# Optimization experiments

Measured on AMD Instinct MI355X. Metric: run time of the kernel, lower is better.

Reference implementation:

```python
import jax, jax.numpy as jnp
import numpy as np

D_MODEL = 1024
N_HEADS = 16
SEQ_LEN = 2048
BATCH = 2
NEG = -1.0e9


def sinusoidal_embeddings(seq_len, d_k):
    # Faithful to the torch version: row 0 is all zeros; even cols get sin,
    # odd cols get cos of position/theta (theta uses the SAME index j, not j//2).
    theta = 10000.0 ** (2.0 * jnp.arange(d_k, dtype=jnp.float32) / d_k)  # [d_k]
    pos = jnp.arange(1, seq_len, dtype=jnp.float32)[:, None] / theta      # [S-1, d_k]
    even = (jnp.arange(d_k) % 2 == 0)
    body = jnp.where(even, jnp.sin(pos), jnp.cos(pos))                    # [S-1, d_k]
    return jnp.concatenate([jnp.zeros((1, d_k), dtype=pos.dtype), body], axis=0)


def setup_inputs() -> dict:
    key = jax.random.key(0)
    k_x, k_q, k_k, k_v, k_o = jax.random.split(key, 5)
    scale = 0.02
    return {
        "X": jax.random.normal(k_x, (BATCH, SEQ_LEN, D_MODEL), dtype=jnp.float32),
        "W_q": jax.random.normal(k_q, (D_MODEL, D_MODEL), dtype=jnp.float32) * scale,
        "W_k": jax.random.normal(k_k, (D_MODEL, D_MODEL), dtype=jnp.float32) * scale,
        "W_v": jax.random.normal(k_v, (D_MODEL, D_MODEL), dtype=jnp.float32) * scale,
        "W_o": jax.random.normal(k_o, (D_MODEL, D_MODEL), dtype=jnp.float32) * scale,
    }


def reference(X, W_q, W_k, W_v, W_o):
    B, S, D = X.shape
    H, d_k = N_HEADS, D // N_HEADS

    def proj(W):  # nn.Linear (no bias): y = x @ W.T, then split heads -> [B,H,S,d_k]
        return (X @ W.T).reshape(B, S, H, d_k).transpose(0, 2, 1, 3)

    Q, K, V = proj(W_q), proj(W_k), proj(W_v)

    pos = sinusoidal_embeddings(S, d_k)          # [S, d_k]
    Q = Q + pos
    K = K + pos

    mask = jnp.triu(jnp.full((S, S), NEG, dtype=X.dtype), k=1)  # [S,S]
    scores = jnp.einsum("bhqd,bhkd->bhqk", Q, K) / jnp.sqrt(jnp.float32(d_k)) + mask
    weights = jax.nn.softmax(scores, axis=-1)
    attn = jnp.einsum("bhqk,bhkd->bhqd", weights, V)            # [B,H,S,d_k]

    attn = attn.transpose(0, 2, 1, 3).reshape(B, S, D)
    return attn @ W_o.T + X
```

## Files before the change

kernel.cpp:

```cpp
#include <hip/hip_runtime.h>
#include <hip/hip_bf16.h>
#include <math.h>

#define S_LEN 2048
#define DMODEL 1024
#define NHEADS 16
#define DHEAD 64
#define NBATCH 2
#define MROWS (NBATCH * S_LEN)

typedef float f32x4 __attribute__((ext_vector_type(4)));
typedef unsigned short u16x8 __attribute__((ext_vector_type(8)));
typedef __bf16 bf16x8 __attribute__((ext_vector_type(8)));

__device__ __forceinline__ f32x4 mfma16(u16x8 a, u16x8 b, f32x4 c) {
    return __builtin_amdgcn_mfma_f32_16x16x32_bf16(
        __builtin_bit_cast(bf16x8, a), __builtin_bit_cast(bf16x8, b), c, 0, 0, 0);
}

__device__ __forceinline__ unsigned short f2bf(float f) {
    unsigned int u = __builtin_bit_cast(unsigned int, f);
    u += 0x7FFFu + ((u >> 16) & 1u);
    return (unsigned short)(u >> 16);
}

__device__ __forceinline__ unsigned int cvtpk(float lo, float hi) {
    unsigned int r;
    asm("v_cvt_pk_bf16_f32 %0, %1, %2" : "=v"(r) : "v"(lo), "v"(hi));
    return r;
}

__device__ __forceinline__ void gl16(const void* g, void* l) {
    __builtin_amdgcn_global_load_lds(
        (const __attribute__((address_space(1))) unsigned int*)g,
        (__attribute__((address_space(3))) unsigned int*)l, 16, 0, 0);
}

#define PIPE_BAR_12() do { \
    asm volatile("s_waitcnt vmcnt(12)" ::: "memory"); \
    __builtin_amdgcn_sched_barrier(0); \
    __builtin_amdgcn_s_barrier(); \
    __builtin_amdgcn_sched_barrier(0); } while (0)
#define PIPE_BAR_0() do { \
    asm volatile("s_waitcnt vmcnt(0)" ::: "memory"); \
    __builtin_amdgcn_sched_barrier(0); \
    __builtin_amdgcn_s_barrier(); \
    __builtin_amdgcn_sched_barrier(0); } while (0)

__global__ __launch_bounds__(256) void cvt5(
    const float* __restrict__ X, const float* __restrict__ Wq,
    const float* __restrict__ Wk, const float* __restrict__ Wv,
    const float* __restrict__ Wo,
    unsigned short* __restrict__ Xbf, unsigned short* __restrict__ Wbf,
    float* __restrict__ pos)
{
    int b = blockIdx.x;
    if (b >= 4096) {
        int i = (b - 4096) * 256 + threadIdx.x;
        int s = i >> 6, d = i & 63;
        float theta = powf(10000.0f, (2.0f * (float)d) / 64.0f);
        float x = (float)s / theta;
        float v = (d & 1) ? cosf(x) : sinf(x);
        pos[i] = (s == 0) ? 0.0f : v;
        return;
    }
    const float* s; unsigned short* d; int t;
    if (b < 2048) { s = X; d = Xbf; t = b * 256 + threadIdx.x; }
    else {
        int z = (b - 2048) >> 9, bb = (b - 2048) & 511;
        s = (z == 0) ? Wq : (z == 1) ? Wk : (z == 2) ? Wv : Wo;
        d = Wbf + (z << 20);
        t = bb * 256 + threadIdx.x;
    }
    float4 a = *((const float4*)s + t * 2);
    float4 c = *((const float4*)s + t * 2 + 1);
    u16x8 o;
    o[0] = f2bf(a.x); o[1] = f2bf(a.y); o[2] = f2bf(a.z); o[3] = f2bf(a.w);
    o[4] = f2bf(c.x); o[5] = f2bf(c.y); o[6] = f2bf(c.z); o[7] = f2bf(c.w);
    *((u16x8*)d + t) = o;
}

__global__ __launch_bounds__(128) void gemm_qkv(
    const unsigned short* __restrict__ Xbf, const unsigned short* __restrict__ Wbf,
    const float* __restrict__ pos,
    unsigned short* __restrict__ qb, unsigned short* __restrict__ kb,
    unsigned short* __restrict__ vt)
{
    const int y = blockIdx.y;
    const int z = y >> 4;
    const unsigned short* __restrict__ W = Wbf + (z << 20);
    __shared__ unsigned short L[3][192 * 64];
    const int t = threadIdx.x;
    const int lane = t & 63;
    const int w = t >> 6;
    const int m0 = blockIdx.x * 128;
    const int n0 = (y & 15) * 64;
    const int ll = lane & 15, lg = lane >> 4;
    const int r8 = lane >> 3, ch = (lane & 7) ^ r8;

    f32x4 acc[4][4] = {};

    const unsigned short* gA[8];
    const unsigned short* gB[4];
    #pragma unroll
    for (int i = 0; i < 8; i++) gA[i] = Xbf + (m0 + w * 64 + i * 8 + r8) * 1024 + ch * 8;
    #pragma unroll
    for (int i = 0; i < 4; i++) gB[i] = W + (n0 + w * 32 + i * 8 + r8) * 1024 + ch * 8;

    const int sw0 = ((0 * 4 + lg) ^ (ll & 7)) * 16;
    const int sw1 = ((1 * 4 + lg) ^ (ll & 7)) * 16;

    auto stage = [&](unsigned short* Lb) {
        unsigned short* const dA = Lb + (w * 64) * 64;
        unsigned short* const dB = Lb + 128 * 64 + (w * 32) * 64;
        #pragma unroll
        for (int i = 0; i < 8; i++) { gl16(gA[i], dA + i * 8 * 64); gA[i] += 64; }
        #pragma unroll
        for (int i = 0; i < 4; i++) { gl16(gB[i], dB + i * 8 * 64); gB[i] += 64; }
    };
    auto compute = [&](const unsigned short* Lb) {
        const char* const pA0 = (const char*)Lb + (w * 64 + ll) * 128 + sw0;
        const char* const pA1 = (const char*)Lb + (w * 64 + ll) * 128 + sw1;
        const char* const pB0 = (const char*)Lb + 16384 + ll * 128 + sw0;
        const char* const pB1 = (const char*)Lb + 16384 + ll * 128 + sw1;
        u16x8 af[4], bfv[4];
        #pragma unroll
        for (int m = 0; m < 4; m++) af[m] = *(const u16x8*)(pA0 + m * 2048);
        #pragma unroll
        for (int n = 0; n < 4; n++) bfv[n] = *(const u16x8*)(pB0 + n * 2048);
        __builtin_amdgcn_s_setprio(1);
        #pragma unroll
        for (int m = 0; m < 4; m++)
            #pragma unroll
            for (int n = 0; n < 4; n++)
                acc[m][n] = mfma16(af[m], bfv[n], acc[m][n]);
        __builtin_amdgcn_s_setprio(0);
        #pragma unroll
        for (int m = 0; m < 4; m++) af[m] = *(const u16x8*)(pA1 + m * 2048);
        #pragma unroll
        for (int n = 0; n < 4; n++) bfv[n] = *(const u16x8*)(pB1 + n * 2048);
        __builtin_amdgcn_s_setprio(1);
        #pragma unroll
        for (int m = 0; m < 4; m++)
            #pragma unroll
            for (int n = 0; n < 4; n++)
                acc[m][n] = mfma16(af[m], bfv[n], acc[m][n]);
        __builtin_amdgcn_s_setprio(0);
    };

    stage(L[0]);
    stage(L[1]);
    PIPE_BAR_12();
    for (int tt = 0; tt < 4; tt++) {
        stage(L[2]); compute(L[0]); PIPE_BAR_12();
        stage(L[0]); compute(L[1]); PIPE_BAR_12();
        stage(L[1]); compute(L[2]); PIPE_BAR_12();
    }
    stage(L[2]); compute(L[0]); PIPE_BAR_12();
    stage(L[0]); compute(L[1]); PIPE_BAR_12();
    compute(L[2]); PIPE_BAR_0();
    compute(L[0]);

    if (z == 2) {
        #pragma unroll
        for (int m = 0; m < 4; m++) {
            const int row0 = m0 + w * 64 + m * 16 + lg * 4;
            const int b = row0 >> 11, s0 = row0 & 2047;
            #pragma unroll
            for (int n = 0; n < 4; n++) {
                const int c = n0 + n * 16 + ll;
                const int h = c >> 6, d = c & 63;
                unsigned long long pk =
                    (unsigned long long)cvtpk(acc[m][n][0], acc[m][n][1]) |
                    ((unsigned long long)cvtpk(acc[m][n][2], acc[m][n][3]) << 32);
                *(unsigned long long*)&vt[(((b * NHEADS + h) * 64) + d) * S_LEN + s0] = pk;
            }
        }
    } else {
        unsigned short* const dst = (z == 0) ? qb : kb;
        #pragma unroll
        for (int m = 0; m < 4; m++) {
            #pragma unroll
            for (int n = 0; n < 4; n++) {
                #pragma unroll
                for (int r = 0; r < 4; r++) {
                    const int row = m0 + w * 64 + m * 16 + lg * 4 + r;
                    const int c = n0 + n * 16 + ll;
                    const int b = row >> 11, s = row & 2047;
                    const int h = c >> 6, d = c & 63;
                    float v = acc[m][n][r] + pos[s * 64 + d];
                    if (z == 0) v *= 0.1803368801111244f;
                    dst[(((b * NHEADS + h) * S_LEN) + s) * 64 + d] = f2bf(v);
                }
            }
        }
    }
}

__global__ __launch_bounds__(512, 4) void attn_kernel(
    const unsigned short* __restrict__ qb,
    const unsigned short* __restrict__ kb,
    const unsigned short* __restrict__ vt,
    unsigned short* __restrict__ attnb)
{
    __shared__ unsigned short Klds[2][64 * 64];
    __shared__ unsigned short Vlds[2][64 * 64];
    __shared__ unsigned short Plds[8][16 * 64];

    const int bh = blockIdx.y;
    const int x = blockIdx.x;
    const int qt = (bh < 16) ? (15 - x) : x;

    const int lane = threadIdx.x & 63;
    const int w = threadIdx.x >> 6;
    const int lg = lane >> 4, ll = lane & 15;
    const int r8 = lane >> 3, ch = (lane & 7) ^ r8;

    const unsigned short* Q = qb + bh * (S_LEN * 64);
    const unsigned short* K = kb + bh * (S_LEN * 64);
    const unsigned short* V = vt + bh * (64 * S_LEN);
    const int q0 = qt * 128 + w * 16;

    u16x8 qf0 = *(const u16x8*)(Q + (q0 + ll) * 64 + lg * 8);
    u16x8 qf1 = *(const u16x8*)(Q + (q0 + ll) * 64 + 32 + lg * 8);

    f32x4 o_acc[4] = {};
    float l_part = 0.0f;

    const int sw0 = ((0 * 4 + lg) ^ (ll & 7)) * 16;
    const int sw1 = ((1 * 4 + lg) ^ (ll & 7)) * 16;
    const int llb = ll * 128;
    const char* k0p0 = (const char*)&Klds[0][0] + llb + sw0;
    const char* k0p1 = (const char*)&Klds[0][0] + llb + sw1;
    const char* k1p0 = (const char*)&Klds[1][0] + llb + sw0;
    const char* k1p1 = (const char*)&Klds[1][0] + llb + sw1;
    const char* v0p0 = (const char*)&Vlds[0][0] + llb + sw0;
    const char* v0p1 = (const char*)&Vlds[0][0] + llb + sw1;
    const char* v1p0 = (const char*)&Vlds[1][0] + llb + sw0;
    const char* v1p1 = (const char*)&Vlds[1][0] + llb + sw1;
    const int E = (ll & 7) << 4;
    char* pwb = (char*)&Plds[w][0] + ((llb + lg * 8) ^ (E & 16));
    const int pw_o0 = 0 ^ (E & 96), pw_o1 = 32 ^ (E & 96);
    const int pw_o2 = 64 ^ (E & 96), pw_o3 = 96 ^ (E & 96);
    const char* pr0 = (const char*)&Plds[w][0] + llb + sw0;
    const char* pr1 = (const char*)&Plds[w][0] + llb + sw1;
    unsigned short* kd0 = &Klds[0][(w * 8) * 64];
    unsigned short* kd1 = &Klds[1][(w * 8) * 64];
    unsigned short* vd0 = &Vlds[0][(w * 8) * 64];
    unsigned short* vd1 = &Vlds[1][(w * 8) * 64];
    const unsigned short* gk = K + (w * 8 + r8) * 64 + ch * 8;
    const unsigned short* gv = V + (w * 8 + r8) * S_LEN + ch * 8;
    const int dthr = w * 16 + ll - lg * 4;

    auto stage2 = [&](unsigned short* kd, unsigned short* vd) {
        gl16(gk, kd);
        gl16(gv, vd);
        gk += 64 * 64;
        gv += 64;
    };

    auto tile_body = [&](const char* kp0, const char* kp1,
                         const char* vp0, const char* vp1, bool masked, int thr) {
        f32x4 sc[4] = {};
        __builtin_amdgcn_s_setprio(1);
        #pragma unroll
        for (int f = 0; f < 4; f++) {
            const u16x8 kfa = *(const u16x8*)(kp0 + f * 2048);
            sc[f] = mfma16(kfa, qf0, sc[f]);
            const u16x8 kfb = *(const u16x8*)(kp1 + f * 2048);
            sc[f] = mfma16(kfb, qf1, sc[f]);
        }
        __builtin_amdgcn_s_setprio(0);
        if (masked) {
            #pragma unroll
            for (int f = 0; f < 4; f++)
                #pragma unroll
                for (int r = 0; r < 4; r++)
                    if (f * 16 + r > thr) sc[f][r] = -1.0e9f;
        }
        float ts = 0.0f;
        #pragma unroll
        for (int f = 0; f < 4; f++)
            #pragma unroll
            for (int r = 0; r < 4; r++) {
                const float p = __builtin_amdgcn_exp2f(sc[f][r]);
                sc[f][r] = p;
                ts += p;
            }
        l_part += ts;
        *(unsigned long long*)(pwb + pw_o0) =
            (unsigned long long)cvtpk(sc[0][0], sc[0][1]) | ((unsigned long long)cvtpk(sc[0][2], sc[0][3]) << 32);
        *(unsigned long long*)(pwb + pw_o1) =
            (unsigned long long)cvtpk(sc[1][0], sc[1][1]) | ((unsigned long long)cvtpk(sc[1][2], sc[1][3]) << 32);
        *(unsigned long long*)(pwb + pw_o2) =
            (unsigned long long)cvtpk(sc[2][0], sc[2][1]) | ((unsigned long long)cvtpk(sc[2][2], sc[2][3]) << 32);
        *(unsigned long long*)(pwb + pw_o3) =
            (unsigned long long)cvtpk(sc[3][0], sc[3][1]) | ((unsigned long long)cvtpk(sc[3][2], sc[3][3]) << 32);
        const u16x8 pf0 = *(const u16x8*)pr0;
        const u16x8 pf1 = *(const u16x8*)pr1;
        __builtin_amdgcn_s_setprio(1);
        #pragma unroll
        for (int f = 0; f < 4; f++) {
            o_acc[f] = mfma16(pf0, *(const u16x8*)(vp0 + f * 2048), o_acc[f]);
            o_acc[f] = mfma16(pf1, *(const u16x8*)(vp1 + f * 2048), o_acc[f]);
        }
        __builtin_amdgcn_s_setprio(0);
    };

    stage2(kd0, vd0);

    for (int p = 0; p < qt; p++) {
        __syncthreads();
        stage2(kd1, vd1);
        tile_body(k0p0, k0p1, v0p0, v0p1, false, 0);
        __syncthreads();
        stage2(kd0, vd0);
        tile_body(k1p0, k1p1, v1p0, v1p1, false, 0);
    }
    __syncthreads();
    stage2(kd1, vd1);
    tile_body(k0p0, k0p1, v0p0, v0p1, true, dthr);
    __syncthreads();
    if (w >= 4)
        tile_body(k1p0, k1p1, v1p0, v1p1, true, dthr - 64);

    l_part += __shfl_xor(l_part, 16);
    l_part += __shfl_xor(l_part, 32);

    const int bb = bh >> 4, h = bh & 15;
    float lr0 = 1.0f / __shfl(l_part, lg * 4 + 0);
    float lr1 = 1.0f / __shfl(l_part, lg * 4 + 1);
    float lr2 = 1.0f / __shfl(l_part, lg * 4 + 2);
    float lr3 = 1.0f / __shfl(l_part, lg * 4 + 3);
    #pragma unroll
    for (int f = 0; f < 4; f++) {
        const int colbase = h * 64 + f * 16 + ll;
        attnb[(bb * S_LEN + q0 + lg * 4 + 0) * DMODEL + colbase] = f2bf(o_acc[f][0] * lr0);
        attnb[(bb * S_LEN + q0 + lg * 4 + 1) * DMODEL + colbase] = f2bf(o_acc[f][1] * lr1);
        attnb[(bb * S_LEN + q0 + lg * 4 + 2) * DMODEL + colbase] = f2bf(o_acc[f][2] * lr2);
        attnb[(bb * S_LEN + q0 + lg * 4 + 3) * DMODEL + colbase] = f2bf(o_acc[f][3] * lr3);
    }
}

__global__ __launch_bounds__(128) void gemm_out(
    const unsigned short* __restrict__ Abf,
    const unsigned short* __restrict__ Wbf,
    const float* __restrict__ X,
    float* __restrict__ out)
{
    const unsigned short* __restrict__ W = Wbf + (3u << 20);
    __shared__ unsigned short L[3][192 * 64];
    const int t = threadIdx.x;
    const int lane = t & 63;
    const int w = t >> 6;
    const int m0 = blockIdx.x * 128;
    const int n0 = blockIdx.y * 64;
    const int ll = lane & 15, lg = lane >> 4;
    const int r8 = lane >> 3, ch = (lane & 7) ^ r8;

    f32x4 acc[4][4] = {};

    const unsigned short* gA[8];
    const unsigned short* gB[4];
    #pragma unroll
    for (int i = 0; i < 8; i++) gA[i] = Abf + (m0 + w * 64 + i * 8 + r8) * 1024 + ch * 8;
    #pragma unroll
    for (int i = 0; i < 4; i++) gB[i] = W + (n0 + w * 32 + i * 8 + r8) * 1024 + ch * 8;

    const int sw0 = ((0 * 4 + lg) ^ (ll & 7)) * 16;
    const int sw1 = ((1 * 4 + lg) ^ (ll & 7)) * 16;

    auto stage = [&](unsigned short* Lb) {
        unsigned short* const dA = Lb + (w * 64) * 64;
        unsigned short* const dB = Lb + 128 * 64 + (w * 32) * 64;
        #pragma unroll
        for (int i = 0; i < 8; i++) { gl16(gA[i], dA + i * 8 * 64); gA[i] += 64; }
        #pragma unroll
        for (int i = 0; i < 4; i++) { gl16(gB[i], dB + i * 8 * 64); gB[i] += 64; }
    };
    auto compute = [&](const unsigned short* Lb) {
        const char* const pA0 = (const char*)Lb + (w * 64 + ll) * 128 + sw0;
        const char* const pA1 = (const char*)Lb + (w * 64 + ll) * 128 + sw1;
        const char* const pB0 = (const char*)Lb + 16384 + ll * 128 + sw0;
        const char* const pB1 = (const char*)Lb + 16384 + ll * 128 + sw1;
        u16x8 af[4], bfv[4];
        #pragma unroll
        for (int m = 0; m < 4; m++) af[m] = *(const u16x8*)(pA0 + m * 2048);
        #pragma unroll
        for (int n = 0; n < 4; n++) bfv[n] = *(const u16x8*)(pB0 + n * 2048);
        __builtin_amdgcn_s_setprio(1);
        #pragma unroll
        for (int m = 0; m < 4; m++)
            #pragma unroll
            for (int n = 0; n < 4; n++)
                acc[m][n] = mfma16(af[m], bfv[n], acc[m][n]);
        __builtin_amdgcn_s_setprio(0);
        #pragma unroll
        for (int m = 0; m < 4; m++) af[m] = *(const u16x8*)(pA1 + m * 2048);
        #pragma unroll
        for (int n = 0; n < 4; n++) bfv[n] = *(const u16x8*)(pB1 + n * 2048);
        __builtin_amdgcn_s_setprio(1);
        #pragma unroll
        for (int m = 0; m < 4; m++)
            #pragma unroll
            for (int n = 0; n < 4; n++)
                acc[m][n] = mfma16(af[m], bfv[n], acc[m][n]);
        __builtin_amdgcn_s_setprio(0);
    };

    stage(L[0]);
    stage(L[1]);
    PIPE_BAR_12();
    for (int tt = 0; tt < 4; tt++) {
        stage(L[2]); compute(L[0]); PIPE_BAR_12();
        stage(L[0]); compute(L[1]); PIPE_BAR_12();
        stage(L[1]); compute(L[2]); PIPE_BAR_12();
    }
    stage(L[2]); compute(L[0]); PIPE_BAR_12();
    stage(L[0]); compute(L[1]); PIPE_BAR_12();
    compute(L[2]); PIPE_BAR_0();
    compute(L[0]);

    #pragma unroll
    for (int m = 0; m < 4; m++)
        #pragma unroll
        for (int n = 0; n < 4; n++)
            #pragma unroll
            for (int r = 0; r < 4; r++) {
                const int row = m0 + w * 64 + m * 16 + lg * 4 + r;
                const int col = n0 + n * 16 + ll;
                out[row * 1024 + col] = acc[m][n][r] + X[row * 1024 + col];
            }
}

extern "C" void kernel_launch(void* const* d_in, const int* in_sizes, int n_in,
                              void* d_out, int out_size, void* d_ws, size_t ws_size,
                              hipStream_t stream) {
    const float* X  = (const float*)d_in[0];
    const float* Wq = (const float*)d_in[1];
    const float* Wk = (const float*)d_in[2];
    const float* Wv = (const float*)d_in[3];
    const float* Wo = (const float*)d_in[4];
    float* out = (float*)d_out;

    char* ws = (char*)d_ws;
    float*          pos  = (float*)(ws);
    unsigned short* Xbf  = (unsigned short*)(ws + (512u << 10));
    unsigned short* Wbf  = (unsigned short*)(ws + (512u << 10) + (8u  << 20));
    unsigned short* qb   = (unsigned short*)(ws + (512u << 10) + (16u << 20));
    unsigned short* kb   = (unsigned short*)(ws + (512u << 10) + (24u << 20));
    unsigned short* vt   = (unsigned short*)(ws + (512u << 10) + (32u << 20));
    unsigned short* attb = Xbf;

    cvt5<<<dim3(4608), dim3(256), 0, stream>>>(X, Wq, Wk, Wv, Wo, Xbf, Wbf, pos);
    gemm_qkv<<<dim3(32, 48), dim3(128), 0, stream>>>(Xbf, Wbf, pos, qb, kb, vt);
    attn_kernel<<<dim3(16, 32), dim3(512), 0, stream>>>(qb, kb, vt, attb);
    gemm_out<<<dim3(32, 16), dim3(128), 0, stream>>>(attb, Wbf, X, out);
}
```

Measured before the change: 102.4 us.

## Stage 128-key K/V tiles per barrier in causal attention kernel

Doubles the K and V shared-memory staging tile from 64 to 128 keys. Each double-buffered stage now loads two 64-key sub-tiles, and the loop advances two stages per iteration, so there are half as many block-wide barriers per key processed. The V layout and global load swizzles are reworked to match the wider transposed tile, and the diagonal and tail cases are restructured. The cost is a larger shared-memory footprint, which can reduce how many blocks fit on a CU.

Measured after the change: 98.61 us. 3.7% less time.

```diff
diff --git a/kernel.cpp b/kernel.cpp
--- a/kernel.cpp
+++ b/kernel.cpp
@@ -203,8 +203,8 @@
     const unsigned short* __restrict__ vt,
     unsigned short* __restrict__ attnb)
 {
-    __shared__ unsigned short Klds[2][64 * 64];
-    __shared__ unsigned short Vlds[2][64 * 64];
+    __shared__ unsigned short Klds[2][128 * 64];
+    __shared__ unsigned short Vlds[2][64 * 128];
     __shared__ unsigned short Plds[8][16 * 64];
 
     const int bh = blockIdx.y;
@@ -215,6 +215,7 @@
     const int w = threadIdx.x >> 6;
     const int lg = lane >> 4, ll = lane & 15;
     const int r8 = lane >> 3, ch = (lane & 7) ^ r8;
+    const int r4 = lane >> 4, c16 = lane & 15;
 
     const unsigned short* Q = qb + bh * (S_LEN * 64);
     const unsigned short* K = kb + bh * (S_LEN * 64);
@@ -229,34 +230,37 @@
 
     const int sw0 = ((0 * 4 + lg) ^ (ll & 7)) * 16;
     const int sw1 = ((1 * 4 + lg) ^ (ll & 7)) * 16;
-    const int llb = ll * 128;
-    const char* k0p0 = (const char*)&Klds[0][0] + llb + sw0;
-    const char* k0p1 = (const char*)&Klds[0][0] + llb + sw1;
-    const char* k1p0 = (const char*)&Klds[1][0] + llb + sw0;
-    const char* k1p1 = (const char*)&Klds[1][0] + llb + sw1;
-    const char* v0p0 = (const char*)&Vlds[0][0] + llb + sw0;
-    const char* v0p1 = (const char*)&Vlds[0][0] + llb + sw1;
-    const char* v1p0 = (const char*)&Vlds[1][0] + llb + sw0;
-    const char* v1p1 = (const char*)&Vlds[1][0] + llb + sw1;
+    const char* kb0p0 = (const char*)&Klds[0][0] + ll * 128 + sw0;
+    const char* kb0p1 = (const char*)&Klds[0][0] + ll * 128 + sw1;
+    const char* kb1p0 = (const char*)&Klds[1][0] + ll * 128 + sw0;
+    const char* kb1p1 = (const char*)&Klds[1][0] + ll * 128 + sw1;
+    const char* vb0p0 = (const char*)&Vlds[0][0] + ll * 256 + sw0;
+    const char* vb0p1 = (const char*)&Vlds[0][0] + ll * 256 + sw1;
+    const char* vb1p0 = (const char*)&Vlds[1][0] + ll * 256 + sw0;
+    const char* vb1p1 = (const char*)&Vlds[1][0] + ll * 256 + sw1;
     const int E = (ll & 7) << 4;
-    char* pwb = (char*)&Plds[w][0] + ((llb + lg * 8) ^ (E & 16));
+    char* pwb = (char*)&Plds[w][0] + (((ll * 128) + lg * 8) ^ (E & 16));
     const int pw_o0 = 0 ^ (E & 96), pw_o1 = 32 ^ (E & 96);
     const int pw_o2 = 64 ^ (E & 96), pw_o3 = 96 ^ (E & 96);
-    const char* pr0 = (const char*)&Plds[w][0] + llb + sw0;
-    const char* pr1 = (const char*)&Plds[w][0] + llb + sw1;
-    unsigned short* kd0 = &Klds[0][(w * 8) * 64];
-    unsigned short* kd1 = &Klds[1][(w * 8) * 64];
-    unsigned short* vd0 = &Vlds[0][(w * 8) * 64];
-    unsigned short* vd1 = &Vlds[1][(w * 8) * 64];
-    const unsigned short* gk = K + (w * 8 + r8) * 64 + ch * 8;
-    const unsigned short* gv = V + (w * 8 + r8) * S_LEN + ch * 8;
+    const char* pr0 = (const char*)&Plds[w][0] + ll * 128 + sw0;
+    const char* pr1 = (const char*)&Plds[w][0] + ll * 128 + sw1;
+    unsigned short* kd0 = &Klds[0][(w * 16) * 64];
+    unsigned short* kd1 = &Klds[1][(w * 16) * 64];
+    unsigned short* vd0 = &Vlds[0][(w * 8) * 128];
+    unsigned short* vd1 = &Vlds[1][(w * 8) * 128];
+    const unsigned short* gk  = K + (w * 16 + r8) * 64 + ch * 8;
+    const unsigned short* gva = V + (w * 8 + r4) * S_LEN + ((c16 ^ r4) * 8);
+    const unsigned short* gvb = V + (w * 8 + 4 + r4) * S_LEN + ((c16 ^ (4 + r4)) * 8);
     const int dthr = w * 16 + ll - lg * 4;
 
     auto stage2 = [&](unsigned short* kd, unsigned short* vd) {
         gl16(gk, kd);
-        gl16(gv, vd);
-        gk += 64 * 64;
-        gv += 64;
+        gl16(gk + 512, kd + 512);
+        gl16(gva, vd);
+        gl16(gvb, vd + 512);
+        gk += 128 * 64;
+        gva += 128;
+        gvb += 128;
     };
 
     auto tile_body = [&](const char* kp0, const char* kp1,
@@ -301,28 +305,45 @@
         __builtin_amdgcn_s_setprio(1);
         #pragma unroll
         for (int f = 0; f < 4; f++) {
-            o_acc[f] = mfma16(pf0, *(const u16x8*)(vp0 + f * 2048), o_acc[f]);
-            o_acc[f] = mfma16(pf1, *(const u16x8*)(vp1 + f * 2048), o_acc[f]);
+            o_acc[f] = mfma16(pf0, *(const u16x8*)(vp0 + f * 4096), o_acc[f]);
+            o_acc[f] = mfma16(pf1, *(const u16x8*)(vp1 + f * 4096), o_acc[f]);
         }
         __builtin_amdgcn_s_setprio(0);
     };
 
+    auto body128_full = [&](const char* kp0, const char* kp1,
+                            const char* vp0, const char* vp1) {
+        tile_body(kp0, kp1, vp0, vp1, false, 0);
+        tile_body(kp0 + 8192, kp1 + 8192, vp0 + 128, vp1 + 128, false, 0);
+    };
+    auto body128_diag = [&](const char* kp0, const char* kp1,
+                            const char* vp0, const char* vp1) {
+        tile_body(kp0, kp1, vp0, vp1, true, dthr);
+        if (w >= 4)
+            tile_body(kp0 + 8192, kp1 + 8192, vp0 + 128, vp1 + 128, true, dthr - 64);
+    };
+
     stage2(kd0, vd0);
-
-    for (int p = 0; p < qt; p++) {
-        __syncthreads();
+    __syncthreads();
+
+    int p = 0;
+    while (p + 2 <= qt) {
         stage2(kd1, vd1);
-        tile_body(k0p0, k0p1, v0p0, v0p1, false, 0);
+        body128_full(kb0p0, kb0p1, vb0p0, vb0p1);
         __syncthreads();
         stage2(kd0, vd0);
-        tile_body(k1p0, k1p1, v1p0, v1p1, false, 0);
-    }
-    __syncthreads();
-    stage2(kd1, vd1);
-    tile_body(k0p0, k0p1, v0p0, v0p1, true, dthr);
-    __syncthreads();
-    if (w >= 4)
-        tile_body(k1p0, k1p1, v1p0, v1p1, true, dthr - 64);
+        body128_full(kb1p0, kb1p1, vb1p0, vb1p1);
+        __syncthreads();
+        p += 2;
+    }
+    if (p < qt) {
+        stage2(kd1, vd1);
+        body128_full(kb0p0, kb0p1, vb0p0, vb0p1);
+        __syncthreads();
+        body128_diag(kb1p0, kb1p1, vb1p0, vb1p1);
+    } else {
+        body128_diag(kb0p0, kb0p1, vb0p0, vb0p1);
+    }
 
     l_part += __shfl_xor(l_part, 16);
     l_part += __shfl_xor(l_part, 32);
```
